# Optimization experiments

Measured on AMD Instinct MI355X. Metric: run time of the kernel, lower is better.

## Reference

```python
import jax, jax.numpy as jnp
import numpy as np

B, S, E, D = 2, 1024, 1024, 2048
H, KV, HD = 8, 4, 256
SOFTCAP = 50.0
SCALE = 256.0 ** -0.5  # query_pre_attn_scalar ** -0.5
WINDOW = 512
EPS = 1e-6
THETA = 10000.0


def setup_inputs() -> dict:
    key = jax.random.key(0)
    ks = jax.random.split(key, 10)
    hidden_states = jax.random.normal(ks[0], (B, S, D), jnp.float32)
    encoder_hidden_states = jax.random.normal(ks[1], (B, E, D), jnp.float32)
    # two packed segments per sequence (position resets at S//2)
    position_ids = jnp.broadcast_to(
        jnp.concatenate([jnp.arange(S // 2), jnp.arange(S - S // 2)]), (B, S)
    ).astype(jnp.int32)
    decoder_attention_mask = jnp.ones((B, S), jnp.int32)
    encoder_attention_mask = jnp.broadcast_to(
        (jnp.arange(E) < (E - 64)).astype(jnp.int32), (B, E))
    # RoPE tables from position ids
    inv_freq = 1.0 / (THETA ** (jnp.arange(0, HD, 2, dtype=jnp.float32) / HD))
    freqs = position_ids.astype(jnp.float32)[..., None] * inv_freq  # [B,S,HD/2]
    emb = jnp.concatenate([freqs, freqs], axis=-1)  # [B,S,HD]
    cos, sin = jnp.cos(emb), jnp.sin(emb)
    wq = 0.02 * jax.random.normal(ks[2], (D, H * HD), jnp.float32)
    wk = 0.02 * jax.random.normal(ks[3], (D, KV * HD), jnp.float32)
    wv = 0.02 * jax.random.normal(ks[4], (D, KV * HD), jnp.float32)
    wo = 0.02 * jax.random.normal(ks[5], (H * HD, D), jnp.float32)
    q_norm_w = 0.1 * jax.random.normal(ks[6], (HD,), jnp.float32)
    k_norm_w = 0.1 * jax.random.normal(ks[7], (HD,), jnp.float32)
    return dict(hidden_states=hidden_states,
                encoder_hidden_states=encoder_hidden_states,
                cos=cos, sin=sin, wq=wq, wk=wk, wv=wv, wo=wo,
                q_norm_w=q_norm_w, k_norm_w=k_norm_w,
                decoder_attention_mask=decoder_attention_mask,
                encoder_attention_mask=encoder_attention_mask,
                position_ids=position_ids)


def _rms_norm(x, w):
    # GemmaRMSNorm: x * rsqrt(mean(x^2)+eps) * (1 + w)
    var = jnp.mean(x * x, axis=-1, keepdims=True)
    return x * jax.lax.rsqrt(var + EPS) * (1.0 + w)


def _rotate_half(x):
    h = x.shape[-1] // 2
    return jnp.concatenate([-x[..., h:], x[..., :h]], axis=-1)


def _build_merged_mask(dec_mask, enc_mask, position_ids):
    dm = dec_mask.astype(bool)
    em = enc_mask.astype(bool)
    Sq = dm.shape[1]
    causal = jnp.tril(jnp.ones((Sq, Sq), bool))
    # segment ids from non-increasing position resets (packing)
    reset = jnp.concatenate(
        [jnp.ones((dm.shape[0], 1), bool),
         position_ids[:, 1:] <= position_ids[:, :-1]], axis=1)
    seg = jnp.cumsum(reset.astype(jnp.int32), axis=1)
    block = seg[:, :, None] == seg[:, None, :]
    full_self = dm[:, None, :] & causal[None] & block  # [B,S,S]
    rows = jnp.arange(Sq)
    dist = rows[:, None] - rows[None, :]
    sliding = (dist >= 0) & (dist < WINDOW)
    self_mask = full_self & sliding[None]
    cross = jnp.broadcast_to(em[:, None, :], (dm.shape[0], Sq, em.shape[1]))
    return jnp.concatenate([self_mask, cross], axis=-1)[:, None]  # [B,1,S,S+E]


def reference(hidden_states, encoder_hidden_states, cos, sin, wq, wk, wv, wo,
              q_norm_w, k_norm_w, decoder_attention_mask,
              encoder_attention_mask, position_ids):
    Bq, Sq, _ = hidden_states.shape
    Ek = encoder_hidden_states.shape[1]
    q = (hidden_states @ wq).reshape(Bq, Sq, H, HD).transpose(0, 2, 1, 3)
    k_self = (hidden_states @ wk).reshape(Bq, Sq, KV, HD).transpose(0, 2, 1, 3)
    v_self = (hidden_states @ wv).reshape(Bq, Sq, KV, HD).transpose(0, 2, 1, 3)
    k_cross = (encoder_hidden_states @ wk).reshape(Bq, Ek, KV, HD).transpose(0, 2, 1, 3)
    v_cross = (encoder_hidden_states @ wv).reshape(Bq, Ek, KV, HD).transpose(0, 2, 1, 3)
    # QK RMSNorm (cross keys normalized but NOT rotated, matching source)
    q = _rms_norm(q, q_norm_w)
    k_self = _rms_norm(k_self, k_norm_w)
    k_cross = _rms_norm(k_cross, k_norm_w)
    c, s = cos[:, None, :, :], sin[:, None, :, :]
    q = q * c + _rotate_half(q) * s
    k_self = k_self * c + _rotate_half(k_self) * s
    k = jnp.concatenate([k_self, k_cross], axis=2)  # [B,KV,S+E,HD]
    v = jnp.concatenate([v_self, v_cross], axis=2)
    rep = H // KV
    k = jnp.repeat(k, rep, axis=1)
    v = jnp.repeat(v, rep, axis=1)
    mask = _build_merged_mask(decoder_attention_mask, encoder_attention_mask,
                              position_ids)
    scores = jnp.einsum('bhqd,bhkd->bhqk', q, k) * SCALE
    scores = SOFTCAP * jnp.tanh(scores / SOFTCAP)  # logit softcapping
    scores = jnp.where(mask, scores, jnp.float32(-1e30))
    attn = jax.nn.softmax(scores, axis=-1)
    out = jnp.einsum('bhqk,bhkd->bhqd', attn, v)
    out = out.transpose(0, 2, 1, 3).reshape(Bq, Sq, H * HD)
    return out @ wo
```

## Files before the change

### kernel.cpp

```cpp
#include <hip/hip_runtime.h>
#include <math.h>

#define B_ 2
#define S_ 1024
#define E_ 1024
#define D_ 2048
#define H_ 8
#define KV_ 4
#define HD_ 256
#define WINDOW_ 512u
#define SCALE_ 0.0625f
#define CAP_ 50.0f
#define EPS_ 1e-6f
#define CROSS_OK (-7)
#define KINV (-2147483647 - 1)

typedef __bf16 bf8_t __attribute__((ext_vector_type(8)));
typedef float fx4 __attribute__((ext_vector_type(4)));
#define MFMA16(a, b, c) __builtin_amdgcn_mfma_f32_16x16x32_bf16((a), (b), (c), 0, 0, 0)

typedef __attribute__((address_space(1))) unsigned int gas_u32;
typedef __attribute__((address_space(3))) unsigned int las_u32;
__device__ __forceinline__ void gl2lds16(const void* g, void* l) {
    __builtin_amdgcn_global_load_lds((const gas_u32*)g, (las_u32*)l, 16, 0, 0);
}

union U4 { __bf16 b[4]; unsigned long long u; };

__device__ __forceinline__ float pexp(float dot) {
    float e = __expf(dot * (2.0f * SCALE_ / CAP_));
    return __expf(-(2.0f * CAP_) / (e + 1.0f));
}

__device__ __forceinline__ void dev_tobf16(const float* __restrict__ x,
                                           __bf16* __restrict__ y, int n4, int i) {
    if (i >= n4) return;
    float4 v = ((const float4*)x)[i];
    U4 p;
    p.b[0] = (__bf16)v.x; p.b[1] = (__bf16)v.y;
    p.b[2] = (__bf16)v.z; p.b[3] = (__bf16)v.w;
    *(unsigned long long*)&y[(size_t)i * 4] = p.u;
}

__device__ __forceinline__ void dev_tsplit(const float* __restrict__ W,
                                           __bf16* __restrict__ Th,
                                           __bf16* __restrict__ Tl, int K, int N,
                                           int bx, int by, int t,
                                           float (*tile)[33], int wlo) {
    const int tx = t & 31, ty = t >> 5;
    const int k0 = bx * 32, n0 = by * 32;
#pragma unroll
    for (int r = 0; r < 4; ++r)
        tile[ty + r * 8][tx] = W[(size_t)(k0 + ty + r * 8) * N + n0 + tx];
    __syncthreads();
#pragma unroll
    for (int r = 0; r < 4; ++r) {
        float v = tile[tx][ty + r * 8];
        __bf16 h = (__bf16)v;
        size_t o = (size_t)(n0 + ty + r * 8) * K + k0 + tx;
        Th[o] = h;
        if (wlo) Tl[o] = (__bf16)(v - (float)h);
    }
}

__device__ __forceinline__ void dev_segscan(const int* __restrict__ pos,
                                            const int* __restrict__ dm,
                                            const int* __restrict__ em,
                                            int* __restrict__ seg,
                                            int* __restrict__ ki,
                                            int b, int t, int* wsum) {
    const int base = b * 1024 + t * 4;
    int4 p = *(const int4*)&pos[base];
    int pm1 = (t == 0) ? 0 : pos[base - 1];
    int r0 = (t == 0) ? 1 : (p.x <= pm1 ? 1 : 0);
    int r1 = (p.y <= p.x), r2 = (p.z <= p.y), r3 = (p.w <= p.z);
    int c0 = r0, c1 = c0 + r1, c2 = c1 + r2, c3 = c2 + r3;
    const int lane = t & 63, wv = t >> 6;
    int x = c3;
#pragma unroll
    for (int off = 1; off < 64; off <<= 1) {
        int y = __shfl_up(x, off, 64);
        if (lane >= off) x += y;
    }
    if (lane == 63) wsum[wv] = x;
    __syncthreads();
    int woff = 0;
#pragma unroll
    for (int w = 0; w < 4; ++w) if (w < wv) woff += wsum[w];
    const int excl = woff + x - c3;
    int sv[4] = {excl + c0, excl + c1, excl + c2, excl + c3};
    int4 dmv = *(const int4*)&dm[base];
    int4 emv = *(const int4*)&em[base];
    int dma[4] = {dmv.x, dmv.y, dmv.z, dmv.w};
    int ema[4] = {emv.x, emv.y, emv.z, emv.w};
#pragma unroll
    for (int r = 0; r < 4; ++r) {
        seg[base + r] = sv[r];
        ki[b * 2048 + t * 4 + r] = dma[r] ? sv[r] : KINV;
        ki[b * 2048 + 1024 + t * 4 + r] = ema[r] ? CROSS_OK : KINV;
    }
}

__global__ __launch_bounds__(256) void prep(
    const float* __restrict__ hs, const float* __restrict__ enc,
    const float* __restrict__ wq, const float* __restrict__ wk,
    const float* __restrict__ wvp, const float* __restrict__ wo,
    const int* __restrict__ pos, const int* __restrict__ dm,
    const int* __restrict__ em,
    __bf16* __restrict__ hs_bf, __bf16* __restrict__ enc_bf,
    __bf16* __restrict__ wqkvTH, __bf16* __restrict__ wqkvTL,
    __bf16* __restrict__ woTH, __bf16* __restrict__ woTL,
    int* __restrict__ seg, int* __restrict__ ki) {
    __shared__ float tile[32][33];
    __shared__ int wsum[4];
    int bid = blockIdx.x;
    const int t = threadIdx.x;
    if (bid < 4096) { dev_tobf16(hs, hs_bf, 1048576, bid * 256 + t); return; }
    bid -= 4096;
    if (bid < 4096) { dev_tobf16(enc, enc_bf, 1048576, bid * 256 + t); return; }
    bid -= 4096;
    if (bid < 4096) {
        dev_tsplit(wq, wqkvTH, nullptr, 2048, 2048, bid & 63, bid >> 6, t, tile, 0);
        return;
    }
    bid -= 4096;
    if (bid < 2048) {
        dev_tsplit(wk, wqkvTH + (size_t)2048 * 2048, nullptr, 2048, 1024,
                   bid & 63, bid >> 6, t, tile, 0);
        return;
    }
    bid -= 2048;
    if (bid < 2048) {
        dev_tsplit(wvp, wqkvTH + (size_t)3072 * 2048, wqkvTL + (size_t)3072 * 2048,
                   2048, 1024, bid & 63, bid >> 6, t, tile, 1);
        return;
    }
    bid -= 2048;
    if (bid < 4096) {
        dev_tsplit(wo, woTH, woTL, 2048, 2048, bid & 63, bid >> 6, t, tile, 1);
        return;
    }
    bid -= 4096;
    dev_segscan(pos, dm, em, seg, ki, bid, t, wsum);
}

template <int NPASS>
__device__ __forceinline__ void gemm_core2(
    const __bf16* __restrict__ Ah, const __bf16* __restrict__ Al,
    const __bf16* __restrict__ Bh, const __bf16* __restrict__ Bl,
    int row0, int col0, int K,
    __bf16* As0, __bf16* As1, __bf16* Bs0, __bf16* Bs1, fx4 (&acc)[4][4]) {
    const int tid = threadIdx.x, lane = tid & 63, wv = tid >> 6;
    const int l15 = lane & 15, lq = lane >> 4;
    const int wm = (wv >> 1) * 64, wn = (wv & 1) * 64;
    constexpr int WCNT = (NPASS == 1) ? 0x0F74 : (NPASS == 2) ? 0x0F76 : 0x0F78;

    auto stage = [&](int buf, int k0) {
#pragma unroll
        for (int s = 0; s < 2; ++s) {
            int ch = (wv * 2 + s) * 64 + lane;
            int r = ch >> 2, cp = ch & 3;
            int cl = (cp - ((r >> 1) & 3)) & 3;
            size_t ga = (size_t)(row0 + r) * K + k0 + cl * 8;
            size_t gb = (size_t)(col0 + r) * K + k0 + cl * 8;
            gl2lds16(Ah + ga, As0 + buf * 4096 + ch * 8);
            if (NPASS >= 3) gl2lds16(Al + ga, As1 + buf * 4096 + ch * 8);
            gl2lds16(Bh + gb, Bs0 + buf * 4096 + ch * 8);
            if (NPASS >= 2) gl2lds16(Bl + gb, Bs1 + buf * 4096 + ch * 8);
        }
    };

    stage(0, 0);
    for (int k0 = 0; k0 < K; k0 += 32) {
        const int buf = (k0 >> 5) & 1;
        const bool hasnext = (k0 + 32 < K);
        if (hasnext) stage(buf ^ 1, k0 + 32);
        if (hasnext) __builtin_amdgcn_s_waitcnt(WCNT);
        else         __builtin_amdgcn_s_waitcnt(0x0F70);
        __builtin_amdgcn_s_barrier();
        __builtin_amdgcn_sched_barrier(0);

        const __bf16* A0 = As0 + buf * 4096;
        const __bf16* A1 = As1 + buf * 4096;
        const __bf16* B0 = Bs0 + buf * 4096;
        const __bf16* B1 = Bs1 + buf * 4096;
        bf8_t ah[4], al[4], bh[4], bl[4];
#pragma unroll
        for (int i = 0; i < 4; ++i) {
            int row = wm + i * 16 + l15;
            int sl = row * 4 + ((lq + (row >> 1)) & 3);
            ah[i] = *(const bf8_t*)(A0 + sl * 8);
            if (NPASS >= 3) al[i] = *(const bf8_t*)(A1 + sl * 8);
        }
#pragma unroll
        for (int j = 0; j < 4; ++j) {
            int row = wn + j * 16 + l15;
            int sl = row * 4 + ((lq + (row >> 1)) & 3);
            bh[j] = *(const bf8_t*)(B0 + sl * 8);
            if (NPASS >= 2) bl[j] = *(const bf8_t*)(B1 + sl * 8);
        }
#pragma unroll
        for (int i = 0; i < 4; ++i)
#pragma unroll
            for (int j = 0; j < 4; ++j) {
                acc[i][j] = MFMA16(ah[i], bh[j], acc[i][j]);
                if (NPASS >= 2) acc[i][j] = MFMA16(ah[i], bl[j], acc[i][j]);
                if (NPASS >= 3) acc[i][j] = MFMA16(al[i], bh[j], acc[i][j]);
            }
        __builtin_amdgcn_sched_barrier(0);
        __builtin_amdgcn_s_barrier();
    }
}

__device__ __forceinline__ void gemm_core_half(
    const __bf16* __restrict__ Ah, const __bf16* __restrict__ Al,
    const __bf16* __restrict__ Bh, const __bf16* __restrict__ Bl,
    int row0, int col0, int K,
    __bf16* As0, __bf16* As1, __bf16* Bs0, __bf16* Bs1, fx4 (&acc)[4][2]) {
    const int tid = threadIdx.x, lane = tid & 63, wv = tid >> 6;
    const int l15 = lane & 15, lq = lane >> 4;
    const int wm = (wv >> 1) * 64, wn = (wv & 1) * 32;

    auto stage = [&](int buf, int k0) {
#pragma unroll
        for (int s = 0; s < 2; ++s) {
            int ch = s * 256 + tid;
            int r = ch >> 2, cp = ch & 3;
            int cl = (cp - ((r >> 1) & 3)) & 3;
            size_t ga = (size_t)(row0 + r) * K + k0 + cl * 8;
            gl2lds16(Ah + ga, As0 + buf * 4096 + ch * 8);
            gl2lds16(Al + ga, As1 + buf * 4096 + ch * 8);
        }
        {
            int ch = tid;
            int r = ch >> 2, cp = ch & 3;
            int cl = (cp - ((r >> 1) & 3)) & 3;
            size_t gb = (size_t)(col0 + r) * K + k0 + cl * 8;
            gl2lds16(Bh + gb, Bs0 + buf * 2048 + ch * 8);
            gl2lds16(Bl + gb, Bs1 + buf * 2048 + ch * 8);
        }
    };

    stage(0, 0);
    for (int k0 = 0; k0 < K; k0 += 32) {
        const int buf = (k0 >> 5) & 1;
        const bool hasnext = (k0 + 32 < K);
        if (hasnext) stage(buf ^ 1, k0 + 32);
        if (hasnext) __builtin_amdgcn_s_waitcnt(0x0F76);
        else         __builtin_amdgcn_s_waitcnt(0x0F70);
        __builtin_amdgcn_s_barrier();
        __builtin_amdgcn_sched_barrier(0);

        const __bf16* A0 = As0 + buf * 4096;
        const __bf16* A1 = As1 + buf * 4096;
        const __bf16* B0 = Bs0 + buf * 2048;
        const __bf16* B1 = Bs1 + buf * 2048;
        bf8_t ah[4], al[4], bh[2], bl[2];
#pragma unroll
        for (int i = 0; i < 4; ++i) {
            int row = wm + i * 16 + l15;
            int sl = row * 4 + ((lq + (row >> 1)) & 3);
            ah[i] = *(const bf8_t*)(A0 + sl * 8);
            al[i] = *(const bf8_t*)(A1 + sl * 8);
        }
#pragma unroll
        for (int j = 0; j < 2; ++j) {
            int row = wn + j * 16 + l15;
            int sl = row * 4 + ((lq + (row >> 1)) & 3);
            bh[j] = *(const bf8_t*)(B0 + sl * 8);
            bl[j] = *(const bf8_t*)(B1 + sl * 8);
        }
#pragma unroll
        for (int i = 0; i < 4; ++i)
#pragma unroll
            for (int j = 0; j < 2; ++j) {
                acc[i][j] = MFMA16(ah[i], bh[j], acc[i][j]);
                acc[i][j] = MFMA16(ah[i], bl[j], acc[i][j]);
                acc[i][j] = MFMA16(al[i], bh[j], acc[i][j]);
            }
        __builtin_amdgcn_sched_barrier(0);
        __builtin_amdgcn_s_barrier();
    }
}

__global__ __launch_bounds__(256) void gemm_proj(
    const __bf16* __restrict__ hsb, const __bf16* __restrict__ encb,
    const __bf16* __restrict__ BTh, const __bf16* __restrict__ BTl,
    float* __restrict__ qf32, float* __restrict__ ksf, float* __restrict__ kcf,
    __bf16* __restrict__ vtS, __bf16* __restrict__ vtC) {
    __shared__ __bf16 As0[8192], Bs0[8192], Bs1[8192];
    const int bx = blockIdx.x, row0 = blockIdx.y * 128;
    const __bf16* A;
    float* Ck; __bf16* Cv; int col0;
    if (bx < 32) { A = hsb;  col0 = bx * 128;               Ck = ksf; Cv = vtS; }
    else         { A = encb; col0 = (bx - 32) * 128 + 2048; Ck = kcf; Cv = vtC; }
    fx4 acc[4][4];
#pragma unroll
    for (int i = 0; i < 4; ++i)
#pragma unroll
        for (int j = 0; j < 4; ++j) acc[i][j] = (fx4){0.f, 0.f, 0.f, 0.f};
    if (col0 >= 3072)
        gemm_core2<2>(A, nullptr, BTh, BTl, row0, col0, D_, As0, nullptr, Bs0, Bs1, acc);
    else
        gemm_core2<1>(A, nullptr, BTh, BTl, row0, col0, D_, As0, nullptr, Bs0, Bs1, acc);

    const int tid = threadIdx.x, lane = tid & 63, wv = tid >> 6;
    const int l15 = lane & 15, lq = lane >> 4;
    const int wm = (wv >> 1) * 64, wn = (wv & 1) * 64;
    const int mode = (col0 < 2048) ? 0 : (col0 < 3072 ? 1 : 2);
#pragma unroll
    for (int i = 0; i < 4; ++i)
#pragma unroll
        for (int j = 0; j < 4; ++j) {
            int mb = row0 + wm + i * 16 + lq * 4;
            int n = col0 + wn + j * 16 + l15;
            if (mode == 0) {
#pragma unroll
                for (int r = 0; r < 4; ++r)
                    qf32[(size_t)(mb + r) * 2048 + n] = acc[i][j][r];
            } else if (mode == 1) {
                int nk = n - 2048;
#pragma unroll
                for (int r = 0; r < 4; ++r)
                    Ck[(size_t)(mb + r) * 1024 + nk] = acc[i][j][r];
            } else {
                int nv = n - 3072;
                int b = mb >> 10, s = mb & 1023;
                int kv = nv >> 8, d = nv & 255;
                U4 pk;
#pragma unroll
                for (int r = 0; r < 4; ++r) pk.b[r] = (__bf16)acc[i][j][r];
                *(unsigned long long*)&Cv[((size_t)(b * KV_ + kv) * HD_ + d) * 1024 + s] = pk.u;
            }
        }
}

__global__ __launch_bounds__(256) void gemm_out(
    const __bf16* __restrict__ Ah, const __bf16* __restrict__ Al,
    const __bf16* __restrict__ Bh, const __bf16* __restrict__ Bl,
    float* __restrict__ C) {
    __shared__ __bf16 As0[8192], As1[8192], Bs0[4096], Bs1[4096];
    const int row0 = blockIdx.y * 128, col0 = blockIdx.x * 64;
    fx4 acc[4][2];
#pragma unroll
    for (int i = 0; i < 4; ++i)
#pragma unroll
        for (int j = 0; j < 2; ++j) acc[i][j] = (fx4){0.f, 0.f, 0.f, 0.f};
    gemm_core_half(Ah, Al, Bh, Bl, row0, col0, 2048, As0, As1, Bs0, Bs1, acc);
    const int tid = threadIdx.x, lane = tid & 63, wv = tid >> 6;
    const int l15 = lane & 15, lq = lane >> 4;
    const int wm = (wv >> 1) * 64, wn = (wv & 1) * 32;
#pragma unroll
    for (int i = 0; i < 4; ++i)
#pragma unroll
        for (int j = 0; j < 2; ++j) {
            int mb = row0 + wm + i * 16 + lq * 4;
            int n = col0 + wn + j * 16 + l15;
#pragma unroll
            for (int r = 0; r < 4; ++r)
                C[(size_t)(mb + r) * 2048 + n] = acc[i][j][r];
        }
}

__global__ __launch_bounds__(256) void rms_all(
    const float* __restrict__ qf32, const float* __restrict__ ksf,
    const float* __restrict__ kcf,
    __bf16* __restrict__ q_bf, __bf16* __restrict__ k_bf,
    __bf16* __restrict__ kc_bf,
    const float* __restrict__ qnw, const float* __restrict__ knw,
    const float* __restrict__ cs, const float* __restrict__ sn) {
    int bid = blockIdx.x;
    const float* x; __bf16* out; const float* w;
    int nheads, do_rope, trans;
    if (bid < 16384)      { x = qf32; out = q_bf;  w = qnw; nheads = 8; do_rope = 1; trans = 0; }
    else if (bid < 24576) { bid -= 16384; x = ksf; out = k_bf;  w = knw; nheads = 4; do_rope = 1; trans = 1; }
    else                  { bid -= 24576; x = kcf; out = kc_bf; w = knw; nheads = 4; do_rope = 0; trans = 1; }
    const int tid = threadIdx.x;
    const size_t base = (size_t)bid * HD_;
    float v = x[base + tid];
    float ss = v * v;
#pragma unroll
    for (int off = 32; off; off >>= 1) ss += __shfl_down(ss, off);
    __shared__ float red[4];
    __shared__ float ybuf[HD_];
    const int lane = tid & 63, wvi = tid >> 6;
    if (lane == 0) red[wvi] = ss;
    __syncthreads();
    float tot = red[0] + red[1] + red[2] + red[3];
    float scale = rsqrtf(tot * (1.0f / HD_) + EPS_);
    float y = v * scale * (1.0f + w[tid]);
    const int m = bid / nheads;
    if (do_rope) {
        ybuf[tid] = y;
        __syncthreads();
        float rot = (tid < HD_ / 2) ? -ybuf[tid + HD_ / 2] : ybuf[tid - HD_ / 2];
        size_t coff = (size_t)m * HD_;
        y = y * cs[coff + tid] + rot * sn[coff + tid];
    }
    size_t oidx;
    if (trans) {
        int hh = bid % nheads;
        int b = m >> 10, s = m & 1023;
        oidx = ((size_t)(b * nheads + hh) * 1024 + s) * HD_ + tid;
    } else {
        oidx = base + tid;
    }
    out[oidx] = (__bf16)y;
}

__global__ __launch_bounds__(256, 1) void attn_part(
    const __bf16* __restrict__ qb,
    const __bf16* __restrict__ kb,
    const __bf16* __restrict__ kcb,
    const __bf16* __restrict__ vtS,
    const __bf16* __restrict__ vtC,
    const int* __restrict__ seg, const int* __restrict__ ki,
    float* __restrict__ accS, float* __restrict__ accC,
    float* __restrict__ lsS, float* __restrict__ lsC) {
    __shared__ __bf16 Ks[2][8192];
    __shared__ __bf16 Vs[2][8192];
    __shared__ __bf16 Ps[4][640];
    __shared__ int kinfoS[1024];
    const int tid = threadIdx.x, lane = tid & 63, wv = tid >> 6;
    const int l15 = lane & 15, lq = lane >> 4;
    const int bid = blockIdx.x;
    const int role = bid >> 8;
    const int g = bid & 7;
    const int b = g >> 2, kv = g & 3;
    const int rest = (bid >> 3) & 31;
    const int qt = rest >> 1, h = kv * 2 + (rest & 1);
    const int s0 = qt * 64;

    int lo = 0, nt = 32;
    const __bf16 *Kbase, *Vbase;
    if (role == 0) {
        lo = (s0 >= 512) ? ((s0 - 511) & ~31) : 0;
        nt = (s0 + 64 - lo) >> 5;
        Kbase = kb + (size_t)(b * KV_ + kv) * (1024 * 256);
        Vbase = vtS + (size_t)(b * KV_ + kv) * (256 * 1024);
    } else {
        Kbase = kcb + (size_t)(b * KV_ + kv) * (1024 * 256);
        Vbase = vtC + (size_t)(b * KV_ + kv) * (256 * 1024);
    }
    const int nk = nt * 32;
    const int kiofs = b * 2048 + (role ? 1024 : lo);
    for (int i = tid; i < nk; i += 256) kinfoS[i] = ki[kiofs + i];
    __syncthreads();

    const int qpos = s0 + wv * 16 + l15;
    bf8_t qf[8];
    const __bf16* qrow = qb + ((size_t)(b * S_ + qpos) * H_ + h) * HD_;
#pragma unroll
    for (int f = 0; f < 8; ++f) qf[f] = *(const bf8_t*)(qrow + f * 32 + lq * 8);
    const int tgt = role ? CROSS_OK : seg[b * S_ + qpos];

    auto stage = [&](int buf, int t) {
        const __bf16* Kt = Kbase + (size_t)(lo + t * 32) * 256;
        const __bf16* Vt = Vbase + (lo + t * 32);
#pragma unroll
        for (int r = 0; r < 4; ++r) {
            int cid = r * 256 + tid;
            int key = cid >> 5, c = cid & 31;
            gl2lds16(Kt + key * 256 + (((c ^ (key & 7))) << 3), &Ks[buf][cid * 8]);
        }
#pragma unroll
        for (int r = 0; r < 4; ++r) {
            int cid = r * 256 + tid;
            int d = cid >> 2, kc = cid & 3;
            gl2lds16(Vt + (size_t)d * 1024 + ((kc ^ ((d >> 1) & 3)) << 3),
                     &Vs[buf][cid * 8]);
        }
    };

    fx4 accO[16];
#pragma unroll
    for (int j = 0; j < 16; ++j) accO[j] = (fx4){0.f, 0.f, 0.f, 0.f};
    float lsum = 0.f;
    const int swzk = l15 & 7;
    const int swzv = lq ^ ((l15 >> 1) & 3);

    stage(0, 0);
    for (int i = 0; i < nt; ++i) {
        const int kt0_c = lo + i * 32;
        const int kio_c = i * 32;
        const bool hasnext = (i + 1 < nt);
        if (hasnext) stage((i + 1) & 1, i + 1);
        if (hasnext) __builtin_amdgcn_s_waitcnt(0x0F78);
        else         __builtin_amdgcn_s_waitcnt(0x0F70);
        __builtin_amdgcn_s_barrier();
        __builtin_amdgcn_sched_barrier(0);

        const __bf16* Ksb = Ks[i & 1];
        const __bf16* Vsb = Vs[i & 1];
        fx4 sc0 = (fx4){0.f, 0.f, 0.f, 0.f}, sc1 = (fx4){0.f, 0.f, 0.f, 0.f};
#pragma unroll
        for (int f = 0; f < 8; ++f) {
            bf8_t k0 = *(const bf8_t*)&Ksb[(l15 * 32 + ((f * 4 + lq) ^ swzk)) * 8];
            bf8_t k1 = *(const bf8_t*)&Ksb[((16 + l15) * 32 + ((f * 4 + lq) ^ swzk)) * 8];
            sc0 = MFMA16(k0, qf[f], sc0);
            sc1 = MFMA16(k1, qf[f], sc1);
        }
        int4 ki0 = *(const int4*)&kinfoS[kio_c + lq * 4];
        int4 ki1 = *(const int4*)&kinfoS[kio_c + 16 + lq * 4];
        int ka0[4] = {ki0.x, ki0.y, ki0.z, ki0.w};
        int ka1[4] = {ki1.x, ki1.y, ki1.z, ki1.w};
        U4 p0, p1;
#pragma unroll
        for (int r = 0; r < 4; ++r) {
            int key0 = kt0_c + lq * 4 + r;
            float e0 = pexp(sc0[r]);
            float e1 = pexp(sc1[r]);
            bool ok0 = (ka0[r] == tgt) && (role || (unsigned)(qpos - key0) < WINDOW_);
            bool ok1 = (ka1[r] == tgt) && (role || (unsigned)(qpos - key0 - 16) < WINDOW_);
            float v0 = ok0 ? e0 : 0.f;
            float v1 = ok1 ? e1 : 0.f;
            lsum += v0 + v1;
            p0.b[r] = (__bf16)v0;
            p1.b[r] = (__bf16)v1;
        }
        *(unsigned long long*)&Ps[wv][l15 * 40 + lq * 4] = p0.u;
        *(unsigned long long*)&Ps[wv][l15 * 40 + 16 + lq * 4] = p1.u;
        bf8_t pf = *(const bf8_t*)&Ps[wv][l15 * 40 + lq * 8];
#pragma unroll
        for (int j = 0; j < 16; ++j) {
            bf8_t vb = *(const bf8_t*)&Vsb[((j * 16 + l15) * 4 + swzv) * 8];
            accO[j] = MFMA16(pf, vb, accO[j]);
        }
        __builtin_amdgcn_sched_barrier(0);
        __builtin_amdgcn_s_barrier();
    }

    lsum += __shfl_xor(lsum, 16, 64);
    lsum += __shfl_xor(lsum, 32, 64);
    float* accT = role ? accC : accS;
    float* lsT  = role ? lsC  : lsS;
    if (lq == 0) lsT[(size_t)(b * S_ + qpos) * 8 + h] = lsum;
#pragma unroll
    for (int j = 0; j < 16; ++j)
#pragma unroll
        for (int r = 0; r < 4; ++r) {
            size_t idx = (size_t)(b * S_ + s0 + wv * 16 + lq * 4 + r) * 2048 +
                         h * 256 + j * 16 + l15;
            accT[idx] = accO[j][r];
        }
}

__global__ __launch_bounds__(256) void combine(
    const float* __restrict__ aS, const float* __restrict__ aC,
    const float* __restrict__ lS, const float* __restrict__ lC,
    __bf16* __restrict__ aH, __bf16* __restrict__ aL) {
    int i = blockIdx.x * 256 + threadIdx.x;
    size_t base = (size_t)i * 4;
    int row = (int)(base >> 11);
    int h = (int)((base >> 8) & 7);
    float inv = 1.0f / (lS[row * 8 + h] + lC[row * 8 + h]);
    float4 a = ((const float4*)aS)[i];
    float4 c = ((const float4*)aC)[i];
    float o[4] = {(a.x + c.x) * inv, (a.y + c.y) * inv,
                  (a.z + c.z) * inv, (a.w + c.w) * inv};
    U4 ph, pl;
#pragma unroll
    for (int r = 0; r < 4; ++r) {
        __bf16 hi = (__bf16)o[r];
        ph.b[r] = hi;
        pl.b[r] = (__bf16)(o[r] - (float)hi);
    }
    *(unsigned long long*)&aH[base] = ph.u;
    *(unsigned long long*)&aL[base] = pl.u;
}

extern "C" void kernel_launch(void* const* d_in, const int* in_sizes, int n_in,
                              void* d_out, int out_size, void* d_ws, size_t ws_size,
                              hipStream_t stream) {
    (void)in_sizes; (void)n_in; (void)out_size; (void)ws_size;
    const float* hs  = (const float*)d_in[0];
    const float* enc = (const float*)d_in[1];
    const float* cs  = (const float*)d_in[2];
    const float* sn  = (const float*)d_in[3];
    const float* wq  = (const float*)d_in[4];
    const float* wk  = (const float*)d_in[5];
    const float* wv  = (const float*)d_in[6];
    const float* wo  = (const float*)d_in[7];
    const float* qnw = (const float*)d_in[8];
    const float* knw = (const float*)d_in[9];
    const int* dm    = (const int*)d_in[10];
    const int* em    = (const int*)d_in[11];
    const int* pos   = (const int*)d_in[12];
    float* out = (float*)d_out;

    char* ws = (char*)d_ws;
    const size_t MB = 1ull << 20;
    __bf16* hs_bf   = (__bf16*)(ws + 0 * MB);
    __bf16* enc_bf  = (__bf16*)(ws + 8 * MB);
    __bf16* wqkvTH  = (__bf16*)(ws + 16 * MB);
    __bf16* wqkvTL  = (__bf16*)(ws + 32 * MB);
    __bf16* woTH    = (__bf16*)(ws + 48 * MB);
    __bf16* woTL    = (__bf16*)(ws + 56 * MB);
    float*  qf32    = (float*)(ws + 64 * MB);
    float*  ksf     = (float*)(ws + 80 * MB);
    float*  kcf     = (float*)(ws + 88 * MB);
    __bf16* k_bf    = (__bf16*)(ws + 104 * MB);
    __bf16* kc_bf   = (__bf16*)(ws + 108 * MB);
    __bf16* vtS     = (__bf16*)(ws + 112 * MB);
    __bf16* vtC     = (__bf16*)(ws + 116 * MB);
    int*    seg     = (int*)(ws + 120 * MB);
    int*    kinfo   = (int*)(ws + 121 * MB);
    __bf16* q_bf    = (__bf16*)(ws + 124 * MB);
    __bf16* aoutH   = (__bf16*)(ws + 0 * MB);
    __bf16* aoutL   = (__bf16*)(ws + 9 * MB);
    float*  accS    = (float*)(ws + 64 * MB);
    float*  accC    = (float*)(ws + 81 * MB);
    float*  lsS     = (float*)(ws + 98 * MB);
    float*  lsC     = (float*)(ws + 99 * MB);

    prep<<<20482, 256, 0, stream>>>(hs, enc, wq, wk, wv, wo, pos, dm, em,
                                    hs_bf, enc_bf, wqkvTH, wqkvTL, woTH, woTL,
                                    seg, kinfo);

    gemm_proj<<<dim3(48, 16), 256, 0, stream>>>(hs_bf, enc_bf, wqkvTH, wqkvTL,
                                                qf32, ksf, kcf, vtS, vtC);

    rms_all<<<32768, 256, 0, stream>>>(qf32, ksf, kcf, q_bf, k_bf, kc_bf,
                                       qnw, knw, cs, sn);

    attn_part<<<512, 256, 0, stream>>>(q_bf, k_bf, kc_bf, vtS, vtC, seg, kinfo,
                                       accS, accC, lsS, lsC);
    combine<<<4096, 256, 0, stream>>>(accS, accC, lsS, lsC, aoutH, aoutL);

    gemm_out<<<dim3(32, 16), 256, 0, stream>>>(aoutH, aoutL, woTH, woTL, out);
}
```

Before: 394.9 us.

## Balance attention blocks by splitting cross-attention tiles between self and cross roles

Load-balances the split attention kernel. Each self-role block now also processes the first part of its cross-attention key tiles, sized so its total tile count is about equal to that of a paired cross-role block, and the cross-role blocks handle the remaining cross tiles. Cross-role blocks walk query tiles in reverse so pairs complement each other. This removes the imbalance where self blocks near the start of the sequence had few tiles while every cross block processed 32. The cost is larger key-info shared memory and slightly more complex per-phase control flow.

```diff
diff --git a/kernel.cpp b/kernel.cpp
--- a/kernel.cpp
+++ b/kernel.cpp
@@ -420,31 +420,37 @@
     __shared__ __bf16 Ks[2][8192];
     __shared__ __bf16 Vs[2][8192];
     __shared__ __bf16 Ps[4][640];
-    __shared__ int kinfoS[1024];
+    __shared__ int kinfoS[1600];
     const int tid = threadIdx.x, lane = tid & 63, wv = tid >> 6;
     const int l15 = lane & 15, lq = lane >> 4;
     const int bid = blockIdx.x;
     const int role = bid >> 8;
     const int g = bid & 7;
     const int b = g >> 2, kv = g & 3;
-    const int rest = (bid >> 3) & 31;
-    const int qt = rest >> 1, h = kv * 2 + (rest & 1);
+    const int idx = (bid >> 3) & 31;
+    const int qt_raw = idx >> 1, h = kv * 2 + (idx & 1);
+    const int qt = role ? (15 - qt_raw) : qt_raw;
     const int s0 = qt * 64;
 
-    int lo = 0, nt = 32;
-    const __bf16 *Kbase, *Vbase;
+    const int lo = (s0 >= 512) ? ((s0 - 511) & ~31) : 0;
+    const int nts = (s0 + 64 - lo) >> 5;
+    const int ccr = (33 - nts) >> 1;
+
+    const __bf16* KbS = kb  + (size_t)(b * KV_ + kv) * (1024 * 256);
+    const __bf16* VbS = vtS + (size_t)(b * KV_ + kv) * (256 * 1024);
+    const __bf16* KbC = kcb + (size_t)(b * KV_ + kv) * (1024 * 256);
+    const __bf16* VbC = vtC + (size_t)(b * KV_ + kv) * (256 * 1024);
+
     if (role == 0) {
-        lo = (s0 >= 512) ? ((s0 - 511) & ~31) : 0;
-        nt = (s0 + 64 - lo) >> 5;
-        Kbase = kb + (size_t)(b * KV_ + kv) * (1024 * 256);
-        Vbase = vtS + (size_t)(b * KV_ + kv) * (256 * 1024);
+        const int nk0 = nts * 32, nk1 = ccr * 32;
+        for (int i = tid; i < nk0; i += 256) kinfoS[i] = ki[b * 2048 + lo + i];
+        for (int i = tid; i < nk1; i += 256)
+            kinfoS[nk0 + i] = ki[b * 2048 + 1024 + i];
     } else {
-        Kbase = kcb + (size_t)(b * KV_ + kv) * (1024 * 256);
-        Vbase = vtC + (size_t)(b * KV_ + kv) * (256 * 1024);
-    }
-    const int nk = nt * 32;
-    const int kiofs = b * 2048 + (role ? 1024 : lo);
-    for (int i = tid; i < nk; i += 256) kinfoS[i] = ki[kiofs + i];
+        const int nk1 = (32 - ccr) * 32;
+        for (int i = tid; i < nk1; i += 256)
+            kinfoS[i] = ki[b * 2048 + 1024 + ccr * 32 + i];
+    }
     __syncthreads();
 
     const int qpos = s0 + wv * 16 + l15;
@@ -452,25 +458,7 @@
     const __bf16* qrow = qb + ((size_t)(b * S_ + qpos) * H_ + h) * HD_;
 #pragma unroll
     for (int f = 0; f < 8; ++f) qf[f] = *(const bf8_t*)(qrow + f * 32 + lq * 8);
-    const int tgt = role ? CROSS_OK : seg[b * S_ + qpos];
-
-    auto stage = [&](int buf, int t) {
-        const __bf16* Kt = Kbase + (size_t)(lo + t * 32) * 256;
-        const __bf16* Vt = Vbase + (lo + t * 32);
-#pragma unroll
-        for (int r = 0; r < 4; ++r) {
-            int cid = r * 256 + tid;
-            int key = cid >> 5, c = cid & 31;
-            gl2lds16(Kt + key * 256 + (((c ^ (key & 7))) << 3), &Ks[buf][cid * 8]);
-        }
-#pragma unroll
-        for (int r = 0; r < 4; ++r) {
-            int cid = r * 256 + tid;
-            int d = cid >> 2, kc = cid & 3;
-            gl2lds16(Vt + (size_t)d * 1024 + ((kc ^ ((d >> 1) & 3)) << 3),
-                     &Vs[buf][cid * 8]);
-        }
-    };
+    const int segq = seg[b * S_ + qpos];
 
     fx4 accO[16];
 #pragma unroll
@@ -479,55 +467,97 @@
     const int swzk = l15 & 7;
     const int swzv = lq ^ ((l15 >> 1) & 3);
 
-    stage(0, 0);
-    for (int i = 0; i < nt; ++i) {
-        const int kt0_c = lo + i * 32;
-        const int kio_c = i * 32;
-        const bool hasnext = (i + 1 < nt);
-        if (hasnext) stage((i + 1) & 1, i + 1);
-        if (hasnext) __builtin_amdgcn_s_waitcnt(0x0F78);
-        else         __builtin_amdgcn_s_waitcnt(0x0F70);
-        __builtin_amdgcn_s_barrier();
-        __builtin_amdgcn_sched_barrier(0);
-
-        const __bf16* Ksb = Ks[i & 1];
-        const __bf16* Vsb = Vs[i & 1];
-        fx4 sc0 = (fx4){0.f, 0.f, 0.f, 0.f}, sc1 = (fx4){0.f, 0.f, 0.f, 0.f};
-#pragma unroll
-        for (int f = 0; f < 8; ++f) {
-            bf8_t k0 = *(const bf8_t*)&Ksb[(l15 * 32 + ((f * 4 + lq) ^ swzk)) * 8];
-            bf8_t k1 = *(const bf8_t*)&Ksb[((16 + l15) * 32 + ((f * 4 + lq) ^ swzk)) * 8];
-            sc0 = MFMA16(k0, qf[f], sc0);
-            sc1 = MFMA16(k1, qf[f], sc1);
-        }
-        int4 ki0 = *(const int4*)&kinfoS[kio_c + lq * 4];
-        int4 ki1 = *(const int4*)&kinfoS[kio_c + 16 + lq * 4];
-        int ka0[4] = {ki0.x, ki0.y, ki0.z, ki0.w};
-        int ka1[4] = {ki1.x, ki1.y, ki1.z, ki1.w};
-        U4 p0, p1;
-#pragma unroll
-        for (int r = 0; r < 4; ++r) {
-            int key0 = kt0_c + lq * 4 + r;
-            float e0 = pexp(sc0[r]);
-            float e1 = pexp(sc1[r]);
-            bool ok0 = (ka0[r] == tgt) && (role || (unsigned)(qpos - key0) < WINDOW_);
-            bool ok1 = (ka1[r] == tgt) && (role || (unsigned)(qpos - key0 - 16) < WINDOW_);
-            float v0 = ok0 ? e0 : 0.f;
-            float v1 = ok1 ? e1 : 0.f;
-            lsum += v0 + v1;
-            p0.b[r] = (__bf16)v0;
-            p1.b[r] = (__bf16)v1;
-        }
-        *(unsigned long long*)&Ps[wv][l15 * 40 + lq * 4] = p0.u;
-        *(unsigned long long*)&Ps[wv][l15 * 40 + 16 + lq * 4] = p1.u;
-        bf8_t pf = *(const bf8_t*)&Ps[wv][l15 * 40 + lq * 8];
-#pragma unroll
-        for (int j = 0; j < 16; ++j) {
-            bf8_t vb = *(const bf8_t*)&Vsb[((j * 16 + l15) * 4 + swzv) * 8];
-            accO[j] = MFMA16(pf, vb, accO[j]);
-        }
-        __builtin_amdgcn_sched_barrier(0);
-        __builtin_amdgcn_s_barrier();
+    const __bf16* phK[2]; const __bf16* phV[2];
+    int phKey0[2], phKio[2], phNt[2], phSelf[2], nph;
+    if (role == 0) {
+        phK[0] = KbS; phV[0] = VbS; phKey0[0] = lo; phKio[0] = 0;
+        phNt[0] = nts; phSelf[0] = 1;
+        phK[1] = KbC; phV[1] = VbC; phKey0[1] = 0; phKio[1] = nts * 32;
+        phNt[1] = ccr; phSelf[1] = 0;
+        nph = 2;
+    } else {
+        phK[0] = KbC; phV[0] = VbC; phKey0[0] = ccr * 32; phKio[0] = 0;
+        phNt[0] = 32 - ccr; phSelf[0] = 0;
+        nph = 1;
+    }
+
+    for (int p = 0; p < nph; ++p) {
+        const __bf16* Kb = phK[p];
+        const __bf16* Vb = phV[p];
+        const int key0 = phKey0[p], kiob = phKio[p], nt = phNt[p];
+        const int selfm = phSelf[p];
+        const int tgt = selfm ? segq : CROSS_OK;
+
+        auto stage = [&](int buf, int t) {
+            const __bf16* Kt = Kb + (size_t)(key0 + t * 32) * 256;
+            const __bf16* Vt = Vb + (key0 + t * 32);
+#pragma unroll
+            for (int r = 0; r < 4; ++r) {
+                int cid = r * 256 + tid;
+                int key = cid >> 5, c = cid & 31;
+                gl2lds16(Kt + key * 256 + (((c ^ (key & 7))) << 3), &Ks[buf][cid * 8]);
+            }
+#pragma unroll
+            for (int r = 0; r < 4; ++r) {
+                int cid = r * 256 + tid;
+                int d = cid >> 2, kc = cid & 3;
+                gl2lds16(Vt + (size_t)d * 1024 + ((kc ^ ((d >> 1) & 3)) << 3),
+                         &Vs[buf][cid * 8]);
+            }
+        };
+
+        stage(0, 0);
+        for (int i = 0; i < nt; ++i) {
+            const int kt0_c = key0 + i * 32;
+            const int kio_c = kiob + i * 32;
+            const bool hasnext = (i + 1 < nt);
+            if (hasnext) stage((i + 1) & 1, i + 1);
+            if (hasnext) __builtin_amdgcn_s_waitcnt(0x0F78);
+            else         __builtin_amdgcn_s_waitcnt(0x0F70);
+            __builtin_amdgcn_s_barrier();
+            __builtin_amdgcn_sched_barrier(0);
+
+            const __bf16* Ksb = Ks[i & 1];
+            const __bf16* Vsb = Vs[i & 1];
+            fx4 sc0 = (fx4){0.f, 0.f, 0.f, 0.f}, sc1 = (fx4){0.f, 0.f, 0.f, 0.f};
+#pragma unroll
+            for (int f = 0; f < 8; ++f) {
+                bf8_t k0 = *(const bf8_t*)&Ksb[(l15 * 32 + ((f * 4 + lq) ^ swzk)) * 8];
+                bf8_t k1 = *(const bf8_t*)&Ksb[((16 + l15) * 32 + ((f * 4 + lq) ^ swzk)) * 8];
+                sc0 = MFMA16(k0, qf[f], sc0);
+                sc1 = MFMA16(k1, qf[f], sc1);
+            }
+            int4 ki0 = *(const int4*)&kinfoS[kio_c + lq * 4];
+            int4 ki1 = *(const int4*)&kinfoS[kio_c + 16 + lq * 4];
+            int ka0[4] = {ki0.x, ki0.y, ki0.z, ki0.w};
+            int ka1[4] = {ki1.x, ki1.y, ki1.z, ki1.w};
+            U4 p0, p1;
+#pragma unroll
+            for (int r = 0; r < 4; ++r) {
+                int key0r = kt0_c + lq * 4 + r;
+                float e0 = pexp(sc0[r]);
+                float e1 = pexp(sc1[r]);
+                bool ok0 = (ka0[r] == tgt) &&
+                           (!selfm || (unsigned)(qpos - key0r) < WINDOW_);
+                bool ok1 = (ka1[r] == tgt) &&
+                           (!selfm || (unsigned)(qpos - key0r - 16) < WINDOW_);
+                float v0 = ok0 ? e0 : 0.f;
+                float v1 = ok1 ? e1 : 0.f;
+                lsum += v0 + v1;
+                p0.b[r] = (__bf16)v0;
+                p1.b[r] = (__bf16)v1;
+            }
+            *(unsigned long long*)&Ps[wv][l15 * 40 + lq * 4] = p0.u;
+            *(unsigned long long*)&Ps[wv][l15 * 40 + 16 + lq * 4] = p1.u;
+            bf8_t pf = *(const bf8_t*)&Ps[wv][l15 * 40 + lq * 8];
+#pragma unroll
+            for (int j = 0; j < 16; ++j) {
+                bf8_t vb = *(const bf8_t*)&Vsb[((j * 16 + l15) * 4 + swzv) * 8];
+                accO[j] = MFMA16(pf, vb, accO[j]);
+            }
+            __builtin_amdgcn_sched_barrier(0);
+            __builtin_amdgcn_s_barrier();
+        }
     }
 
     lsum += __shfl_xor(lsum, 16, 64);
@@ -539,9 +569,9 @@
     for (int j = 0; j < 16; ++j)
 #pragma unroll
         for (int r = 0; r < 4; ++r) {
-            size_t idx = (size_t)(b * S_ + s0 + wv * 16 + lq * 4 + r) * 2048 +
-                         h * 256 + j * 16 + l15;
-            accT[idx] = accO[j][r];
+            size_t idx2 = (size_t)(b * S_ + s0 + wv * 16 + lq * 4 + r) * 2048 +
+                          h * 256 + j * 16 + l15;
+            accT[idx2] = accO[j][r];
         }
 }
 
```

Result: no change. 388.5 us (-1.6%).
